# Performance work log

Hardware: AMD Instinct MI355X
Metric: run time of the kernel (lower is better)

Reference implementation:

```python
import jax, jax.numpy as jnp
import numpy as np

BS, IN_DIM, OUT_DIM, N_MASKS = 512, 784, 1024, 16


def setup_inputs() -> dict:
    key = jax.random.key(0)
    k_x, k_s, k_m, k_k, k_b = jax.random.split(key, 5)
    x = jax.random.normal(k_x, (BS, IN_DIM), dtype=jnp.float32)
    state = jax.random.randint(k_s, (BS, 1), 0, N_MASKS, dtype=jnp.int32)
    # binary connectivity masks, one per ordering/state (MADE-style)
    masks = jax.random.bernoulli(k_m, 0.5, (N_MASKS, IN_DIM, OUT_DIM)).astype(jnp.float32)
    # RandomNormal(mean=0, stddev=0.1) initializers from build()
    kernel = 0.1 * jax.random.normal(k_k, (IN_DIM, OUT_DIM), dtype=jnp.float32)
    b_0 = 0.1 * jax.random.normal(k_b, (1, OUT_DIM), dtype=jnp.float32)
    return {"x": x, "state": state, "masks": masks, "kernel": kernel, "b_0": b_0}


def reference(x, state, masks, kernel, b_0):
    # gather per-sample mask: [bs, in_dim, out_dim]
    m = masks[state.reshape(-1)]
    # out[b,o] = sum_i x[b,i] * kernel[i,o] * m[b,i,o]  (masked per-sample matmul)
    out = jnp.einsum('bi,io,bio->bo', x, kernel, m) + b_0
    return jax.nn.relu(out)
```

## Files before the change

kernel.cpp:

```cpp
#include <hip/hip_runtime.h>
#include <hip/hip_bf16.h>


#define IN_DIM 784
#define OUT_DIM 1024
#define BS 512

typedef __attribute__((ext_vector_type(8))) short bf16x8;
typedef __attribute__((ext_vector_type(16))) float f32x16;

static __device__ inline short f2bf(float f) {
    __hip_bfloat16 h = __float2bfloat16(f);
    short r; __builtin_memcpy(&r, &h, 2); return r;
}

static __device__ inline void gload_lds16(const float* g, float* lds_base_uniform) {
    __builtin_amdgcn_global_load_lds(
        (const __attribute__((address_space(1))) void*)g,
        (__attribute__((address_space(3))) void*)lds_base_uniform, 16, 0, 0);
}

static __device__ inline bf16x8 pack8(float4 a, float4 b) {
    bf16x8 r;
    r[0]=f2bf(a.x); r[1]=f2bf(a.y); r[2]=f2bf(a.z); r[3]=f2bf(a.w);
    r[4]=f2bf(b.x); r[5]=f2bf(b.y); r[6]=f2bf(b.z); r[7]=f2bf(b.w);
    return r;
}

__global__ __launch_bounds__(512, 2) void made_fused(
    const float* __restrict__ x,
    const int*   __restrict__ state,
    const float* __restrict__ masks,
    const float* __restrict__ kern,
    const float* __restrict__ bias,
    float*       __restrict__ out)
{
    __shared__ float tiles[2][2][64][32];
    __shared__ int   list[BS];
    __shared__ int   cnt;

    const int tid  = threadIdx.x;
    const int lane = tid & 63;
    const int w    = tid >> 6;
    const int q    = w & 3;
    const int m    = w >> 2;
    const int bid  = blockIdx.x;
    const int s    = bid >> 5;
    const int ot   = bid & 31;
    const int oc0  = ot * 32;

    const int l31 = lane & 31, khl = lane >> 5;
    const float* mS = masks + (size_t)s * IN_DIM * OUT_DIM;

    auto stageF = [&](int t, int b) {
        const int slot = w * 64 + lane;
        const int row  = slot >> 3, ch = slot & 7;
        const size_t go = (size_t)(t * 64 + row) * OUT_DIM + oc0 + ch * 4;
        gload_lds16(kern + go, &tiles[b][0][0][0] + (size_t)w * 64 * 4);
        gload_lds16(mS   + go, &tiles[b][1][0][0] + (size_t)w * 64 * 4);
    };
    auto stageT = [&](int b) {
        if (w < 4) {
            const int wi   = w & 1;
            const int slot = wi * 64 + lane;
            const int row  = slot >> 3, ch = slot & 7;
            const size_t go = (size_t)(768 + row) * OUT_DIM + oc0 + ch * 4;
            const float* src = (w < 2) ? kern + go : mS + go;
            float* dst = (w < 2) ? &tiles[b][0][0][0] + (size_t)wi * 64 * 4
                                 : &tiles[b][1][0][0] + (size_t)wi * 64 * 4;
            gload_lds16(src, dst);
        }
    };

    stageF(0, 0);
    if (tid == 0) cnt = 0;
    __syncthreads();
    { int st = state[tid]; if (st == s) { int p = atomicAdd(&cnt, 1); list[p] = tid; } }
    __syncthreads();
    const int ns = cnt;

    float (*red)[3][16][64] = (float (*)[3][16][64])tiles;

    for (int mb = 0; mb < ns; mb += 64) {
        int r0 = mb + m * 32 + l31; if (r0 >= ns) r0 = ns - 1;
        const float* xr = x + (size_t)list[r0] * IN_DIM;
        bf16x8 a[13];
#pragma unroll
        for (int t = 0; t < 12; ++t) {
            const int off = t * 64 + q * 16 + khl * 8;
            a[t] = pack8(*(const float4*)(xr + off), *(const float4*)(xr + off + 4));
        }
        a[12] = pack8(*(const float4*)(xr + 768 + khl * 8),
                      *(const float4*)(xr + 772 + khl * 8));

        f32x16 acc;
#pragma unroll
        for (int r = 0; r < 16; ++r) acc[r] = 0.f;

        int cb = 0;
        for (int t = 0; t < 13; ++t) {
            if (t + 1 < 12)      stageF(t + 1, cb ^ 1);
            else if (t + 1 == 12) stageT(cb ^ 1);
            if (t < 12) {
                bf16x8 bfr;
#pragma unroll
                for (int e = 0; e < 8; ++e) {
                    const int row = q * 16 + khl * 8 + e;
                    bfr[e] = f2bf(tiles[cb][0][row][l31] * tiles[cb][1][row][l31]);
                }
                acc = __builtin_amdgcn_mfma_f32_32x32x16_bf16(a[t], bfr, acc, 0, 0, 0);
            } else if (q == 0) {
                bf16x8 bfr;
#pragma unroll
                for (int e = 0; e < 8; ++e) {
                    const int row = khl * 8 + e;
                    bfr[e] = f2bf(tiles[cb][0][row][l31] * tiles[cb][1][row][l31]);
                }
                acc = __builtin_amdgcn_mfma_f32_32x32x16_bf16(a[12], bfr, acc, 0, 0, 0);
            }
            __syncthreads();
            cb ^= 1;
        }

        if (q) {
#pragma unroll
            for (int j = 0; j < 16; ++j) red[m][q - 1][j][lane] = acc[j];
        }
        __syncthreads();
        if (q == 0) {
            const float bv = bias[oc0 + l31];
#pragma unroll
            for (int j = 0; j < 16; ++j) {
                float v = acc[j] + red[m][0][j][lane] + red[m][1][j][lane]
                                 + red[m][2][j][lane];
                const int row = (j & 3) + 8 * (j >> 2) + 4 * khl;
                const int sr  = mb + m * 32 + row;
                if (sr < ns) {
                    float o = v + bv;
                    out[(size_t)list[sr] * OUT_DIM + oc0 + l31] = o > 0.f ? o : 0.f;
                }
            }
        }
        __syncthreads();
        if (mb + 64 < ns) stageF(0, 0);
        __syncthreads();
    }
}

extern "C" void kernel_launch(void* const* d_in, const int* in_sizes, int n_in,
                              void* d_out, int out_size, void* d_ws, size_t ws_size,
                              hipStream_t stream) {
    (void)in_sizes; (void)n_in; (void)out_size; (void)d_ws; (void)ws_size;
    const float* x     = (const float*)d_in[0];
    const int*   state = (const int*)  d_in[1];
    const float* masks = (const float*)d_in[2];
    const float* kern  = (const float*)d_in[3];
    const float* b0    = (const float*)d_in[4];
    float* out = (float*)d_out;

    made_fused<<<dim3(512), dim3(512), 0, stream>>>(x, state, masks, kern, b0, out);
}
```

Measured before the change: 32.21 us.

## Triple-buffer kernel/mask tiles with explicit vmcnt waits and unrolled K loop

Replaces the double-buffered LDS staging with a three-stage ring, prefetching two tiles ahead and using explicit s_waitcnt vmcnt plus a raw s_barrier instead of __syncthreads after each step. The K loop is fully unrolled, the tail tile is unified into the same stage function, bias is hoisted, and inactive row halves skip MFMA work. Launch bounds are raised to 4 blocks per CU. This is meant to hide global-to-LDS latency and reduce barrier cost, at the price of more LDS per block and tighter register limits.

```diff
diff --git a/kernel.cpp b/kernel.cpp
--- a/kernel.cpp
+++ b/kernel.cpp
@@ -27,7 +27,7 @@
     return r;
 }
 
-__global__ __launch_bounds__(512, 2) void made_fused(
+__global__ __launch_bounds__(512, 4) void made_fused2(
     const float* __restrict__ x,
     const int*   __restrict__ state,
     const float* __restrict__ masks,
@@ -35,7 +35,7 @@
     const float* __restrict__ bias,
     float*       __restrict__ out)
 {
-    __shared__ float tiles[2][2][64][32];
+    __shared__ float tiles[3][2][64][32];
     __shared__ int   list[BS];
     __shared__ int   cnt;
 
@@ -48,40 +48,32 @@
     const int s    = bid >> 5;
     const int ot   = bid & 31;
     const int oc0  = ot * 32;
+    const int l31  = lane & 31, khl = lane >> 5;
 
-    const int l31 = lane & 31, khl = lane >> 5;
     const float* mS = masks + (size_t)s * IN_DIM * OUT_DIM;
 
-    auto stageF = [&](int t, int b) {
-        const int slot = w * 64 + lane;
-        const int row  = slot >> 3, ch = slot & 7;
-        const size_t go = (size_t)(t * 64 + row) * OUT_DIM + oc0 + ch * 4;
-        gload_lds16(kern + go, &tiles[b][0][0][0] + (size_t)w * 64 * 4);
-        gload_lds16(mS   + go, &tiles[b][1][0][0] + (size_t)w * 64 * 4);
-    };
-    auto stageT = [&](int b) {
-        if (w < 4) {
-            const int wi   = w & 1;
-            const int slot = wi * 64 + lane;
-            const int row  = slot >> 3, ch = slot & 7;
-            const size_t go = (size_t)(768 + row) * OUT_DIM + oc0 + ch * 4;
-            const float* src = (w < 2) ? kern + go : mS + go;
-            float* dst = (w < 2) ? &tiles[b][0][0][0] + (size_t)wi * 64 * 4
-                                 : &tiles[b][1][0][0] + (size_t)wi * 64 * 4;
-            gload_lds16(src, dst);
-        }
-    };
-
-    stageF(0, 0);
     if (tid == 0) cnt = 0;
     __syncthreads();
     { int st = state[tid]; if (st == s) { int p = atomicAdd(&cnt, 1); list[p] = tid; } }
     __syncthreads();
     const int ns = cnt;
 
+    const float biasv = bias[oc0 + l31];
+    asm volatile("" :: "v"(biasv));
+
+    auto stage = [&](int t, int b) {
+        const int r  = w * 8 + (lane >> 3);
+        const int gr = (t == 12) ? 768 + (r & 15) : t * 64 + r;
+        const size_t go = (size_t)gr * OUT_DIM + oc0 + (lane & 7) * 4;
+        gload_lds16(kern + go, &tiles[b][0][w * 8][0]);
+        gload_lds16(mS   + go, &tiles[b][1][w * 8][0]);
+    };
+
     float (*red)[3][16][64] = (float (*)[3][16][64])tiles;
 
     for (int mb = 0; mb < ns; mb += 64) {
+        const bool active = (mb + m * 32) < ns;
+
         int r0 = mb + m * 32 + l31; if (r0 >= ns) r0 = ns - 1;
         const float* xr = x + (size_t)list[r0] * IN_DIM;
         bf16x8 a[13];
@@ -97,38 +89,38 @@
 #pragma unroll
         for (int r = 0; r < 16; ++r) acc[r] = 0.f;
 
-        int cb = 0;
+        stage(0, 0);
+        stage(1, 1);
+        __builtin_amdgcn_sched_barrier(0);
+
+#pragma unroll
         for (int t = 0; t < 13; ++t) {
-            if (t + 1 < 12)      stageF(t + 1, cb ^ 1);
-            else if (t + 1 == 12) stageT(cb ^ 1);
-            if (t < 12) {
+            if (t + 1 < 13) stage(t + 1, (t + 1) % 3);
+            if (t < 12) asm volatile("s_waitcnt vmcnt(2)" ::: "memory");
+            else        asm volatile("s_waitcnt vmcnt(0)" ::: "memory");
+            __builtin_amdgcn_sched_barrier(0);
+            __builtin_amdgcn_s_barrier();
+            __builtin_amdgcn_sched_barrier(0);
+
+            const int buf = t % 3;
+            if (active && (t < 12 || q == 0)) {
                 bf16x8 bfr;
 #pragma unroll
                 for (int e = 0; e < 8; ++e) {
-                    const int row = q * 16 + khl * 8 + e;
-                    bfr[e] = f2bf(tiles[cb][0][row][l31] * tiles[cb][1][row][l31]);
+                    const int row = ((t < 12) ? q * 16 : 0) + khl * 8 + e;
+                    bfr[e] = f2bf(tiles[buf][0][row][l31] * tiles[buf][1][row][l31]);
                 }
                 acc = __builtin_amdgcn_mfma_f32_32x32x16_bf16(a[t], bfr, acc, 0, 0, 0);
-            } else if (q == 0) {
-                bf16x8 bfr;
-#pragma unroll
-                for (int e = 0; e < 8; ++e) {
-                    const int row = khl * 8 + e;
-                    bfr[e] = f2bf(tiles[cb][0][row][l31] * tiles[cb][1][row][l31]);
-                }
-                acc = __builtin_amdgcn_mfma_f32_32x32x16_bf16(a[12], bfr, acc, 0, 0, 0);
             }
-            __syncthreads();
-            cb ^= 1;
         }
 
-        if (q) {
+        __syncthreads();
+        if (q && active) {
 #pragma unroll
             for (int j = 0; j < 16; ++j) red[m][q - 1][j][lane] = acc[j];
         }
         __syncthreads();
-        if (q == 0) {
-            const float bv = bias[oc0 + l31];
+        if (q == 0 && active) {
 #pragma unroll
             for (int j = 0; j < 16; ++j) {
                 float v = acc[j] + red[m][0][j][lane] + red[m][1][j][lane]
@@ -136,13 +128,11 @@
                 const int row = (j & 3) + 8 * (j >> 2) + 4 * khl;
                 const int sr  = mb + m * 32 + row;
                 if (sr < ns) {
-                    float o = v + bv;
+                    float o = v + biasv;
                     out[(size_t)list[sr] * OUT_DIM + oc0 + l31] = o > 0.f ? o : 0.f;
                 }
             }
         }
-        __syncthreads();
-        if (mb + 64 < ns) stageF(0, 0);
         __syncthreads();
     }
 }
@@ -158,5 +148,5 @@
     const float* b0    = (const float*)d_in[4];
     float* out = (float*)d_out;
 
-    made_fused<<<dim3(512), dim3(512), 0, stream>>>(x, state, masks, kern, b0, out);
+    made_fused2<<<dim3(512), dim3(512), 0, stream>>>(x, state, masks, kern, b0, out);
 }
```

After: 44.04 us. 1.37x slower.
